# Kernel tuning notes

Hardware: AMD Instinct MI355X
Metric: run time of the kernel (lower is better)

Reference implementation:

```python
import jax, jax.numpy as jnp
import numpy as np

_FIRST_DECODE_ID = 0  # _T5_DECODER_START_TOKEN_ID
B, L, V = 1, 520, 32128
REVIEW_INDEX = 512
LENIENCY = 2


def setup_inputs() -> dict:
    key = jax.random.key(0)
    k1, k2, k3 = jax.random.split(key, 3)
    target_logits = jax.random.normal(k1, (B, L, V), dtype=jnp.float32)
    probs = jax.random.uniform(k2, (B, L, V), dtype=jnp.float32)
    input_ids = jax.random.randint(k3, (B, L), 0, V, dtype=jnp.int64)
    return {
        "target_logits": target_logits,
        "probs": probs,
        "input_ids": input_ids,
        "review_index": REVIEW_INDEX,
        "leniency": LENIENCY,
    }


def reference(target_logits, probs, input_ids, review_index, leniency):
    r = int(review_index)
    L = input_ids.shape[1]
    K = L - r  # number of draft tokens under review

    target_probs = jax.nn.softmax(target_logits, axis=-1)          # (1, L, V)
    argmax_ids = jnp.argmax(target_probs, axis=-1)                  # (1, L)
    first = jnp.full((1, 1), _FIRST_DECODE_ID, dtype=input_ids.dtype)
    target_ids = jnp.concatenate([first, argmax_ids.astype(input_ids.dtype)], axis=-1)[:, r:]  # (1, K+1)
    target_probs_s = target_probs[:, r - 1:, :]                     # (1, K+1, V)
    probs_new = probs[:, r - 1:, :]                                 # (1, K+1, V)
    draft_ids = input_ids[:, r:]                                    # (1, K)

    # verification flags (fused replacement of the python early-exit loop)
    eq = target_ids[:, :K] == draft_ids                             # (1, K)
    tp = jnp.take_along_axis(target_probs_s[:, :K, :], draft_ids[..., None], axis=-1)[..., 0]
    pp = jnp.take_along_axis(probs_new[:, :K, :], draft_ids[..., None], axis=-1)[..., 0]
    lenient = (leniency > 1) & (tp > pp / jnp.float32(leniency))
    accept = eq | lenient                                           # (1, K)
    # n_match = length of leading run of accepts == match_ct in the loop
    n_match = jnp.sum(jnp.cumprod(accept.astype(jnp.int32), axis=-1))

    # id_res: prefix (r) + accepted drafts (n_match) + 1 bonus target token, padded to r+K+1
    pos = jnp.arange(K + 1)
    draft_pad = jnp.pad(draft_ids, ((0, 0), (0, 1)))                # (1, K+1)
    new_ids = jnp.where(pos < n_match, draft_pad[0],
                        jnp.where(pos == n_match, target_ids[0], 0))
    id_res = jnp.concatenate([input_ids[0, :r], new_ids])[None, :]  # (1, r+K+1)

    # prob_res: probs[:, :r] ++ target_probs of accepted positions, zero-padded to r+K
    mask = (jnp.arange(K) < n_match)[:, None]
    new_probs = jnp.where(mask, target_probs_s[0, :K, :], jnp.float32(0.0))
    prob_res = jnp.concatenate([probs[0, :r, :], new_probs], axis=0)[None]  # (1, r+K, V)

    return id_res, prob_res, n_match
```

## Files before the change

kernel.cpp:

```cpp
#include <hip/hip_runtime.h>
#include <hip/hip_bf16.h>


#define NCHUNK 32
#define BLK 256
#define NSTATS ((8 + 1) * NCHUNK)
#define GRID1 2048
#define NCOPY (GRID1 - NSTATS - 1)

struct Ws {
    float pmax[16][NCHUNK];
    float psum[16][NCHUNK];
    int   pidx[16][NCHUNK];
};

struct MIS { float m; int i; float s; };

__device__ inline MIS mis_merge(MIS a, MIS b) {
    MIS r;
    r.i = (b.m > a.m || (b.m == a.m && b.i < a.i)) ? b.i : a.i;
    r.m = fmaxf(a.m, b.m);
    r.s = 0.0f;
    if (a.s > 0.0f) r.s += a.s * expf(a.m - r.m);
    if (b.s > 0.0f) r.s += b.s * expf(b.m - r.m);
    return r;
}

typedef float f4 __attribute__((ext_vector_type(4)));

__global__ __launch_bounds__(BLK)
void fused_copy_stats(const float* __restrict__ logits,
                      const float* __restrict__ probs,
                      const int* __restrict__ ids,
                      float* __restrict__ out, Ws* __restrict__ ws,
                      int V, int r, long long prob_off, int nf4) {
    int t = threadIdx.x;
    int b = blockIdx.x;

    if (b < NSTATS) {
        int ch = b & (NCHUNK - 1);
        int j  = b / NCHUNK;
        int chunk_elems = V / NCHUNK;
        int cf4 = chunk_elems / 4;
        int cbase = ch * chunk_elems;
        const float4* row = (const float4*)(logits + (size_t)(r - 1 + j) * V + cbase);

        float m = -INFINITY, s = 0.0f;
        int   mi = 0x7fffffff;
        for (int f = t; f < cf4; f += BLK) {
            float4 v = row[f];
            float vv[4] = {v.x, v.y, v.z, v.w};
            int c = cbase + f * 4;
            #pragma unroll
            for (int u = 0; u < 4; u++) {
                float x = vv[u];
                if (x > m) { s = s * expf(m - x) + 1.0f; m = x; mi = c + u; }
                else       { s += expf(x - m); }
            }
        }

        __shared__ float sm[BLK];
        __shared__ int   si[BLK];
        __shared__ float ss[BLK];
        sm[t] = m; si[t] = mi; ss[t] = s;
        __syncthreads();
        for (int w = BLK >> 1; w > 0; w >>= 1) {
            if (t < w) {
                MIS a = {sm[t], si[t], ss[t]};
                MIS bb = {sm[t + w], si[t + w], ss[t + w]};
                MIS rr = mis_merge(a, bb);
                sm[t] = rr.m; si[t] = rr.i; ss[t] = rr.s;
            }
            __syncthreads();
        }
        if (t == 0) {
            ws->pmax[j][ch] = sm[0];
            ws->psum[j][ch] = ss[0];
            ws->pidx[j][ch] = si[0];
        }
        return;
    }

    if (b < NSTATS + NCOPY) {
        int cb   = b - NSTATS;
        int lane = t & 63;
        int wave = cb * (BLK / 64) + (t >> 6);
        const int NW = NCOPY * (BLK / 64);
        int per = (nf4 + NW - 1) / NW;
        per = (per + 63) & ~63;
        long long f0 = (long long)wave * per;
        long long f1 = f0 + per; if (f1 > nf4) f1 = nf4;

        const f4* src4 = (const f4*)probs;
        float* dstB = out + prob_off + 3;
        for (long long f = f0 + lane; f < f1; f += 64) {
            f4 v = src4[f + 1];
            float pw = __shfl_up(v.w, 1);
            if (lane == 0) pw = probs[4 * f + 3];
            f4 o; o.x = pw; o.y = v.x; o.z = v.y; o.w = v.z;
            __builtin_nontemporal_store(o, reinterpret_cast<f4*>(dstB + 4 * f));
        }
        return;
    }

    for (int i = t; i < r; i += BLK) out[i] = (float)ids[i];
    if (t < 3)       out[prob_off + t] = probs[t];
    else if (t == 3) {
        long long last = (long long)r * V - 1;
        out[prob_off + last] = probs[last];
    }
}

#define TP_EPT 8
typedef float f4u __attribute__((ext_vector_type(4), aligned(4)));

__global__ __launch_bounds__(BLK)
void tail_kernel(const float* __restrict__ logits, const float* __restrict__ probs,
                 const int* __restrict__ ids, const int* __restrict__ leniency_p,
                 float* __restrict__ out, const Ws* __restrict__ ws,
                 int V, int r, int K, long long prob_off, long long out_last) {
    __shared__ float s_mx[12];
    __shared__ float s_sum[12];
    __shared__ int   s_amax[12];
    __shared__ int   s_draft[12];
    __shared__ int   s_acc[12];
    __shared__ int   s_nm;
    int t = threadIdx.x;
    int j   = blockIdx.y;
    int sub = blockIdx.x;

    if (t <= K) {
        MIS acc = {ws->pmax[t][0], ws->pidx[t][0], ws->psum[t][0]};
        for (int c = 1; c < NCHUNK; c++) {
            MIS bb = {ws->pmax[t][c], ws->pidx[t][c], ws->psum[t][c]};
            acc = mis_merge(acc, bb);
        }
        s_mx[t] = acc.m; s_sum[t] = acc.s; s_amax[t] = acc.i;
    }
    __syncthreads();

    if (t < K) {
        int dj = ids[r + t];
        s_draft[t] = dj;
        size_t rowoff = (size_t)(r - 1 + t) * V;
        float tp = expf(logits[rowoff + dj] - s_mx[t]) / s_sum[t];
        float pp = probs[rowoff + dj];
        int   len = *leniency_p;
        bool eq      = (s_amax[t] == dj);
        bool lenient = (len > 1) && (tp > pp / (float)len);
        s_acc[t] = (eq || lenient) ? 1 : 0;
    }
    __syncthreads();

    if (t == 0) {
        int nm = 0;
        for (int q = 0; q < K; q++) { if (s_acc[q]) nm++; else break; }
        s_nm = nm;
    }
    __syncthreads();
    int nm = s_nm;

    if (j == 0 && sub == 0) {
        if (t <= K) {
            int v;
            if (t < nm)       v = s_draft[t];
            else if (t == nm) v = s_amax[t];
            else              v = 0;
            out[r + t] = (float)v;
        }
        if (t == K + 1) out[out_last] = (float)nm;
    }

    long long ob = prob_off + (long long)(r + j) * V;
    const float* lg = logits + (size_t)(r - 1 + j) * V;
    bool on = (j < nm);
    float m   = s_mx[j];
    float inv = on ? (1.0f / s_sum[j]) : 0.0f;

    if (sub == 0) {
        if (t < 3)       out[ob + t]     = on ? expf(lg[t] - m) * inv : 0.0f;
        else if (t == 3) out[ob + V - 1] = on ? expf(lg[V - 1] - m) * inv : 0.0f;
    }
    int nf4r = (V - 4) / 4;
    float* dst = out + ob + 3;
    const float* srcl = lg + 3;
    #pragma unroll
    for (int k = 0; k < TP_EPT; k++) {
        int i = sub * (BLK * TP_EPT) + t + k * BLK;
        if (i < nf4r) {
            f4 v;
            if (on) {
                f4u x = *reinterpret_cast<const f4u*>(srcl + 4 * (size_t)i);
                v.x = expf(x.x - m) * inv; v.y = expf(x.y - m) * inv;
                v.z = expf(x.z - m) * inv; v.w = expf(x.w - m) * inv;
            } else {
                v = (f4)0.0f;
            }
            __builtin_nontemporal_store(v, reinterpret_cast<f4*>(dst + 4 * (size_t)i));
        }
    }
}

extern "C" void kernel_launch(void* const* d_in, const int* in_sizes, int n_in,
                              void* d_out, int out_size, void* d_ws, size_t ws_size,
                              hipStream_t stream) {
    const float* logits     = (const float*)d_in[0];
    const float* probs      = (const float*)d_in[1];
    const int*   ids        = (const int*)d_in[2];
    const int*   leniency_p = (const int*)d_in[4];
    float* out = (float*)d_out;
    Ws*    ws  = (Ws*)d_ws;

    const int L = in_sizes[2];
    const int V = in_sizes[0] / L;
    const int r = 512;
    const int K = L - r;
    const long long prob_off = (long long)r + K + 1;
    const long long out_last = (long long)out_size - 1;

    const long long N = (long long)r * V;
    const int nf4 = (int)((N - 3) / 4);

    fused_copy_stats<<<GRID1, BLK, 0, stream>>>(logits, probs, ids, out, ws,
                                                V, r, prob_off, nf4);

    dim3 g2((V / 4 + BLK * TP_EPT - 1) / (BLK * TP_EPT), K, 1);
    tail_kernel<<<g2, BLK, 0, stream>>>(logits, probs, ids, leniency_p, out, ws,
                                        V, r, K, prob_off, out_last);
}
```

Before: 34.88 us.

## Spread probs copy across all blocks including stats blocks, unroll copy loop 4x

Every block now takes part in the shifted probs copy. Blocks that first compute per-chunk softmax stats afterwards copy a smaller chunk (448 float4 per wave), and the remaining blocks copy 512 each. The separate copy-only blocks are gone. The copy inner loop is unrolled to issue four 16-byte loads per lane before the stores, raising memory-level parallelism. This balances load between stats blocks and copy blocks, at the cost of longer stats blocks. A fixed chunk partition that depends on the grid size could leave data uncovered if sizes change.

```diff
diff --git a/kernel.cpp b/kernel.cpp
--- a/kernel.cpp
+++ b/kernel.cpp
@@ -6,7 +6,9 @@
 #define BLK 256
 #define NSTATS ((8 + 1) * NCHUNK)
 #define GRID1 2048
-#define NCOPY (GRID1 - NSTATS - 1)
+#define SWAVES (NSTATS * (BLK / 64))
+#define CH_S 448
+#define CH_C 512
 
 struct Ws {
     float pmax[16][NCHUNK];
@@ -34,6 +36,9 @@
                       const int* __restrict__ ids,
                       float* __restrict__ out, Ws* __restrict__ ws,
                       int V, int r, long long prob_off, int nf4) {
+    __shared__ float sm[BLK];
+    __shared__ int   si[BLK];
+    __shared__ float ss[BLK];
     int t = threadIdx.x;
     int b = blockIdx.x;
 
@@ -58,10 +63,6 @@
                 else       { s += expf(x - m); }
             }
         }
-
-        __shared__ float sm[BLK];
-        __shared__ int   si[BLK];
-        __shared__ float ss[BLK];
         sm[t] = m; si[t] = mi; ss[t] = s;
         __syncthreads();
         for (int w = BLK >> 1; w > 0; w >>= 1) {
@@ -78,36 +79,63 @@
             ws->psum[j][ch] = ss[0];
             ws->pidx[j][ch] = si[0];
         }
-        return;
-    }
-
-    if (b < NSTATS + NCOPY) {
-        int cb   = b - NSTATS;
-        int lane = t & 63;
-        int wave = cb * (BLK / 64) + (t >> 6);
-        const int NW = NCOPY * (BLK / 64);
-        int per = (nf4 + NW - 1) / NW;
-        per = (per + 63) & ~63;
-        long long f0 = (long long)wave * per;
-        long long f1 = f0 + per; if (f1 > nf4) f1 = nf4;
-
-        const f4* src4 = (const f4*)probs;
-        float* dstB = out + prob_off + 3;
-        for (long long f = f0 + lane; f < f1; f += 64) {
-            f4 v = src4[f + 1];
-            float pw = __shfl_up(v.w, 1);
-            if (lane == 0) pw = probs[4 * f + 3];
-            f4 o; o.x = pw; o.y = v.x; o.z = v.y; o.w = v.z;
-            __builtin_nontemporal_store(o, reinterpret_cast<f4*>(dstB + 4 * f));
-        }
-        return;
-    }
-
-    for (int i = t; i < r; i += BLK) out[i] = (float)ids[i];
-    if (t < 3)       out[prob_off + t] = probs[t];
-    else if (t == 3) {
-        long long last = (long long)r * V - 1;
-        out[prob_off + last] = probs[last];
+    } else if (b == GRID1 - 1) {
+        for (int i = t; i < r; i += BLK) out[i] = (float)ids[i];
+        if (t < 3)       out[prob_off + t] = probs[t];
+        else if (t == 3) {
+            long long last = (long long)r * V - 1;
+            out[prob_off + last] = probs[last];
+        }
+    }
+
+    int lane = t & 63;
+    int w = b * (BLK / 64) + (t >> 6);
+    long long f0, len;
+    if (w < SWAVES) { f0 = (long long)w * CH_S;                            len = CH_S; }
+    else            { f0 = (long long)SWAVES * CH_S + (long long)(w - SWAVES) * CH_C; len = CH_C; }
+    long long fend = f0 + len;
+    if (fend > nf4) fend = nf4;
+    if (f0 >= fend) return;
+
+    const f4* src4 = (const f4*)probs;
+    float* dstB = out + prob_off + 3;
+
+    long long g = f0;
+    for (; g + 256 <= fend; g += 256) {
+        long long fA = g + lane;
+        f4 v0 = src4[fA + 1];
+        f4 v1 = src4[fA + 65];
+        f4 v2 = src4[fA + 129];
+        f4 v3 = src4[fA + 193];
+        float p0 = __shfl_up(v0.w, 1);
+        float p1 = __shfl_up(v1.w, 1);
+        float p2 = __shfl_up(v2.w, 1);
+        float p3 = __shfl_up(v3.w, 1);
+        if (lane == 0) {
+            p0 = probs[4 * g + 3];
+            p1 = probs[4 * (g + 64) + 3];
+            p2 = probs[4 * (g + 128) + 3];
+            p3 = probs[4 * (g + 192) + 3];
+        }
+        f4 o0 = {p0, v0.x, v0.y, v0.z};
+        f4 o1 = {p1, v1.x, v1.y, v1.z};
+        f4 o2 = {p2, v2.x, v2.y, v2.z};
+        f4 o3 = {p3, v3.x, v3.y, v3.z};
+        __builtin_nontemporal_store(o0, reinterpret_cast<f4*>(dstB + 4 * fA));
+        __builtin_nontemporal_store(o1, reinterpret_cast<f4*>(dstB + 4 * (fA + 64)));
+        __builtin_nontemporal_store(o2, reinterpret_cast<f4*>(dstB + 4 * (fA + 128)));
+        __builtin_nontemporal_store(o3, reinterpret_cast<f4*>(dstB + 4 * (fA + 192)));
+    }
+    for (; g < fend; g += 64) {
+        long long fA = g + lane;
+        bool ok = fA < fend;
+        f4 v = ok ? src4[fA + 1] : (f4){0.0f, 0.0f, 0.0f, 0.0f};
+        float pw = __shfl_up(v.w, 1);
+        if (lane == 0) pw = probs[4 * g + 3];
+        if (ok) {
+            f4 o = {pw, v.x, v.y, v.z};
+            __builtin_nontemporal_store(o, reinterpret_cast<f4*>(dstB + 4 * fA));
+        }
     }
 }
 
```

New measurement: 33.28 us. 1.05x faster.
